# Optimization experiments

Hardware: AMD Instinct MI355X
Metric: run time of the kernel (lower is better)

Reference implementation:

```python
import jax, jax.numpy as jnp
import numpy as np
from jax import lax

N = 100000      # number of nodes (== ninput)
E = 3200000     # number of edges per adjacency
NHID = 128
EPS = 1e-12     # torch F.normalize eps


def spmm(src, dst, w, x):
    # sparse adj @ x : out[i] = sum_{e: dst[e]==i} w[e] * x[src[e]]
    return jax.ops.segment_sum(w[:, None] * x[src], dst, num_segments=N)


def l2norm(x):
    # F.normalize(x, p=2, dim=1)
    n = jnp.sqrt(jnp.sum(x * x, axis=1, keepdims=True))
    return x / jnp.maximum(n, EPS)


def mlp(x, L1, bl1, L2, bl2, L3, bl3):
    # dropout == 0.0 -> identity; chunking is a memory optimization, same math
    h = jax.nn.relu(x @ L1 + bl1)
    h = jax.nn.relu(h @ L2 + bl2)
    return h @ L3 + bl3  # [N, 1]


def setup_inputs() -> dict:
    key = jax.random.key(0)
    ks = jax.random.split(key, 32)
    d = {}
    d["adj1_src"] = jax.random.randint(ks[0], (E,), 0, N, dtype=jnp.int32)
    d["adj1_dst"] = jax.random.randint(ks[1], (E,), 0, N, dtype=jnp.int32)
    d["adj1_w"] = jax.random.uniform(ks[2], (E,), dtype=jnp.float32)
    d["adj2_src"] = jax.random.randint(ks[3], (E,), 0, N, dtype=jnp.int32)
    d["adj2_dst"] = jax.random.randint(ks[4], (E,), 0, N, dtype=jnp.int32)
    d["adj2_w"] = jax.random.uniform(ks[5], (E,), dtype=jnp.float32)
    d["W1"] = jax.random.normal(ks[6], (N, NHID), dtype=jnp.float32) * 0.05
    d["b1"] = jnp.zeros((NHID,), jnp.float32)
    for i, k in zip(range(2, 7), ks[7:12]):
        d[f"W{i}"] = jax.random.normal(k, (NHID, NHID), dtype=jnp.float32) * (1.0 / np.sqrt(NHID))
        d[f"b{i}"] = jnp.zeros((NHID,), jnp.float32)
    d["L1"] = jax.random.normal(ks[12], (NHID, 2 * NHID), dtype=jnp.float32) * (1.0 / np.sqrt(NHID))
    d["bl1"] = jnp.zeros((2 * NHID,), jnp.float32)
    d["L2"] = jax.random.normal(ks[13], (2 * NHID, 2 * NHID), dtype=jnp.float32) * (1.0 / np.sqrt(2 * NHID))
    d["bl2"] = jnp.zeros((2 * NHID,), jnp.float32)
    d["L3"] = jax.random.normal(ks[14], (2 * NHID, 1), dtype=jnp.float32) * (1.0 / np.sqrt(2 * NHID))
    d["bl3"] = jnp.zeros((1,), jnp.float32)
    return d


def reference(adj1_src, adj1_dst, adj1_w, adj2_src, adj2_dst, adj2_w,
              W1, b1, W2, b2, W3, b3, W4, b4, W5, b5, W6, b6,
              L1, bl1, L2, bl2, L3, bl3):
    def branch(src, dst, w):
        x1 = l2norm(jax.nn.relu(spmm(src, dst, w, W1) + b1))
        x2 = l2norm(jax.nn.relu(spmm(src, dst, w, x1 @ W2) + b2))
        x3 = l2norm(jax.nn.relu(spmm(src, dst, w, x2 @ W3) + b3))
        x4 = l2norm(jax.nn.relu(spmm(src, dst, w, x3 @ W4) + b4))
        x5 = l2norm(jax.nn.relu(spmm(src, dst, w, x4 @ W5) + b5))
        x6 = jax.nn.relu(spmm(src, dst, w, x5 @ W6) + b6)
        x7 = lax.stop_gradient(x1 + x2 + x3 + x4 + x5 + x6)  # .detach()
        s = jnp.zeros((N, 1), jnp.float32)
        for xi in (x1, x2, x3, x4, x5):  # computed under torch.no_grad()
            s = s + lax.stop_gradient(mlp(xi, L1, bl1, L2, bl2, L3, bl3))
        s = s + mlp(x6, L1, bl1, L2, bl2, L3, bl3)
        s = s + mlp(x7, L1, bl1, L2, bl2, L3, bl3)
        return s / 7.0

    score1 = branch(adj1_src, adj1_dst, adj1_w)
    score2 = branch(adj2_src, adj2_dst, adj2_w)
    return score1 * score2
```

## Files before the change

### kernel.cpp

```cpp
#include <hip/hip_runtime.h>

#define NN 100000
#define NE 3200000
#define HID 128
#define NNH ((size_t)NN * HID)

typedef __attribute__((ext_vector_type(8))) _Float16 f16x8;
typedef __attribute__((ext_vector_type(4))) _Float16 f16x4;
typedef __attribute__((ext_vector_type(4))) float f32x4;

#define SWZ(row, k) ((k) ^ (((row) & 7) << 3))

__global__ void zero_k(int* p, int n) {
    int i = blockIdx.x * 256 + threadIdx.x;
    if (i < n) p[i] = 0;
}

__global__ void hist_k(const int* __restrict__ dst, int* __restrict__ cnt) {
    int e = blockIdx.x * 256 + threadIdx.x;
    if (e < NE) atomicAdd(&cnt[dst[e]], 1);
}

__global__ __launch_bounds__(1024) void scanA_k(int* __restrict__ rowptr, int* __restrict__ bsum, int n) {
    __shared__ int wsum[16];
    int tid = threadIdx.x;
    int lane = tid & 63, wid = tid >> 6;
    int idx = blockIdx.x * 1024 + tid;
    int v = (idx < n) ? rowptr[idx] : 0;
    int s = v;
#pragma unroll
    for (int o = 1; o < 64; o <<= 1) {
        int t = __shfl_up(s, o, 64);
        if (lane >= o) s += t;
    }
    if (lane == 63) wsum[wid] = s;
    __syncthreads();
    if (wid == 0) {
        int ws = (lane < 16) ? wsum[lane] : 0;
#pragma unroll
        for (int o = 1; o < 16; o <<= 1) {
            int t = __shfl_up(ws, o, 64);
            if (lane >= o) ws += t;
        }
        if (lane < 16) wsum[lane] = ws;
    }
    __syncthreads();
    int woff = (wid == 0) ? 0 : wsum[wid - 1];
    if (idx < n) rowptr[idx] = woff + s - v;
    if (tid == 0) bsum[blockIdx.x] = wsum[15];
}

__global__ void scanB_k(int* __restrict__ bsum, int* __restrict__ rowptr, int nb, int n) {
    if (threadIdx.x == 0) {
        int run = 0;
        for (int i = 0; i < nb; ++i) {
            int t = bsum[i];
            bsum[i] = run;
            run += t;
        }
        rowptr[n] = run;
    }
}

__global__ void scanC_k(int* __restrict__ rowptr, int* __restrict__ cursor,
                        const int* __restrict__ bsum, int n) {
    int idx = blockIdx.x * 256 + threadIdx.x;
    if (idx < n) {
        int v = rowptr[idx] + bsum[idx >> 10];
        rowptr[idx] = v;
        cursor[idx] = v;
    }
}

__global__ void scatter_k(const int* __restrict__ src, const int* __restrict__ dst,
                          const float* __restrict__ w, int* __restrict__ cursor,
                          unsigned* __restrict__ ep) {
    int e = blockIdx.x * 256 + threadIdx.x;
    if (e < NE) {
        int d = dst[e];
        int pos = atomicAdd(&cursor[d], 1);
        ushort hb = __builtin_bit_cast(ushort, (_Float16)w[e]);
        ep[pos] = ((unsigned)src[e] << 15) | (unsigned)hb;
    }
}

__global__ void convT_k(const float* __restrict__ W, _Float16* __restrict__ WT, int K, int N) {
    int idx = blockIdx.x * 256 + threadIdx.x;
    if (idx < K * N) {
        int k = idx / N, n = idx % N;
        WT[n * K + k] = (_Float16)W[idx];
    }
}

__global__ void conv4_k(const float* __restrict__ A, _Float16* __restrict__ B, int n4) {
    int i = blockIdx.x * 256 + threadIdx.x;
    if (i < n4) {
        float4 v = ((const float4*)A)[i];
        f16x4 h;
        h.x = (_Float16)v.x; h.y = (_Float16)v.y; h.z = (_Float16)v.z; h.w = (_Float16)v.w;
        ((f16x4*)B)[i] = h;
    }
}

template <bool EPI>
__global__ void spmm_k(const _Float16* __restrict__ x, const int* __restrict__ rowptr,
                       const unsigned* __restrict__ ep, const float* __restrict__ bias,
                       _Float16* __restrict__ outx) {
    int row = blockIdx.x * 4 + (threadIdx.x >> 6);
    int l = threadIdx.x & 63;
    int q = l >> 4, li = l & 15;
    if (row >= NN) return;
    int e0 = rowptr[row], e1 = rowptr[row + 1];
    float acc[8] = {};
#pragma unroll 4
    for (int e = e0 + q; e < e1; e += 4) {
        unsigned r = ep[e];
        int s = r >> 15;
        float w = (float)__builtin_bit_cast(_Float16, (ushort)(r & 0x7FFFu));
        f16x8 v = *(const f16x8*)(x + (size_t)s * HID + li * 8);
#pragma unroll
        for (int j = 0; j < 8; ++j) acc[j] += w * (float)v[j];
    }
#pragma unroll
    for (int j = 0; j < 8; ++j) {
        acc[j] += __shfl_xor(acc[j], 16, 64);
        acc[j] += __shfl_xor(acc[j], 32, 64);
    }
    if (EPI) {
        const float4* bp = (const float4*)(bias + li * 8);
        float4 b0 = bp[0], b1 = bp[1];
        acc[0] = fmaxf(acc[0] + b0.x, 0.f); acc[1] = fmaxf(acc[1] + b0.y, 0.f);
        acc[2] = fmaxf(acc[2] + b0.z, 0.f); acc[3] = fmaxf(acc[3] + b0.w, 0.f);
        acc[4] = fmaxf(acc[4] + b1.x, 0.f); acc[5] = fmaxf(acc[5] + b1.y, 0.f);
        acc[6] = fmaxf(acc[6] + b1.z, 0.f); acc[7] = fmaxf(acc[7] + b1.w, 0.f);
        float ss = 0.f;
#pragma unroll
        for (int j = 0; j < 8; ++j) ss += acc[j] * acc[j];
        ss += __shfl_xor(ss, 1, 64);
        ss += __shfl_xor(ss, 2, 64);
        ss += __shfl_xor(ss, 4, 64);
        ss += __shfl_xor(ss, 8, 64);
        float sc = 1.0f / fmaxf(sqrtf(ss), 1e-12f);
#pragma unroll
        for (int j = 0; j < 8; ++j) acc[j] *= sc;
    }
    if (q == 0) {
        f16x8 ho;
#pragma unroll
        for (int j = 0; j < 8; ++j) ho[j] = (_Float16)acc[j];
        *(f16x8*)(outx + (size_t)row * HID + li * 8) = ho;
    }
}

template <bool NORM>
__global__ __launch_bounds__(256) void trans_mlp_k(
    const _Float16* __restrict__ Y,
    const _Float16* __restrict__ WT,
    const float* __restrict__ bw,
    _Float16* __restrict__ Xo,
    const _Float16* __restrict__ L1T, const float* __restrict__ bl1,
    const _Float16* __restrict__ L2T, const float* __restrict__ bl2,
    const float* __restrict__ L3, const float* __restrict__ bl3,
    float* __restrict__ sacc) {
    __shared__ _Float16 Xs[64][128];
    __shared__ _Float16 H1s[64][256];
    __shared__ float red[4][64];
    int t = threadIdx.x;
    int w = t >> 6, l = t & 63;
    int g = l >> 4, li = l & 15;
    int rowBase = blockIdx.x * 64;

#pragma unroll
    for (int i = 0; i < 4; ++i) {
        int idx = t + i * 256;
        int r = idx >> 4, c8 = idx & 15;
        int gr = rowBase + r;
        f16x8 v = (gr < NN) ? *(const f16x8*)(Y + (size_t)gr * 128 + c8 * 8)
                            : (f16x8)(_Float16)0.f;
        *(f16x8*)&Xs[r][SWZ(r, c8 * 8)] = v;
    }
    __syncthreads();

    int cW = w * 32;
    f32x4 accw[4][2] = {};
#pragma unroll
    for (int ks = 0; ks < 4; ++ks) {
        int kb = ks * 32 + g * 8;
        f16x8 a[4];
#pragma unroll
        for (int mt = 0; mt < 4; ++mt) {
            int r = mt * 16 + li;
            a[mt] = *(const f16x8*)&Xs[r][SWZ(r, kb)];
        }
#pragma unroll
        for (int nt = 0; nt < 2; ++nt) {
            f16x8 b = *(const f16x8*)(WT + (size_t)(cW + nt * 16 + li) * 128 + kb);
#pragma unroll
            for (int mt = 0; mt < 4; ++mt)
                accw[mt][nt] = __builtin_amdgcn_mfma_f32_16x16x32_f16(a[mt], b, accw[mt][nt], 0, 0, 0);
        }
    }
    float vv[4][2][4];
    float b0 = bw[cW + li], b1v = bw[cW + 16 + li];
#pragma unroll
    for (int mt = 0; mt < 4; ++mt)
#pragma unroll
        for (int r4 = 0; r4 < 4; ++r4) {
            vv[mt][0][r4] = fmaxf(accw[mt][0][r4] + b0, 0.f);
            vv[mt][1][r4] = fmaxf(accw[mt][1][r4] + b1v, 0.f);
        }
    if (NORM) {
#pragma unroll
        for (int mt = 0; mt < 4; ++mt)
#pragma unroll
            for (int r4 = 0; r4 < 4; ++r4) {
                float ps = vv[mt][0][r4] * vv[mt][0][r4] + vv[mt][1][r4] * vv[mt][1][r4];
                ps += __shfl_xor(ps, 1, 64);
                ps += __shfl_xor(ps, 2, 64);
                ps += __shfl_xor(ps, 4, 64);
                ps += __shfl_xor(ps, 8, 64);
                if (li == 0) red[w][mt * 16 + g * 4 + r4] = ps;
            }
        __syncthreads();
        if (t < 64) {
            float s = red[0][t] + red[1][t] + red[2][t] + red[3][t];
            red[0][t] = 1.f / fmaxf(sqrtf(s), 1e-12f);
        }
        __syncthreads();
    } else {
        __syncthreads();
    }
#pragma unroll
    for (int mt = 0; mt < 4; ++mt)
#pragma unroll
        for (int r4 = 0; r4 < 4; ++r4) {
            int row = mt * 16 + g * 4 + r4;
            float sc = NORM ? red[0][row] : 1.f;
            _Float16 h0 = (_Float16)(vv[mt][0][r4] * sc);
            _Float16 h1 = (_Float16)(vv[mt][1][r4] * sc);
            Xs[row][SWZ(row, cW + li)] = h0;
            Xs[row][SWZ(row, cW + 16 + li)] = h1;
            int gr = rowBase + row;
            if (gr < NN) {
                Xo[(size_t)gr * 128 + cW + li] = h0;
                Xo[(size_t)gr * 128 + cW + 16 + li] = h1;
            }
        }
    __syncthreads();

    int cM = w * 64;
    f32x4 acc[4][4] = {};
#pragma unroll
    for (int ks = 0; ks < 4; ++ks) {
        int kb = ks * 32 + g * 8;
        f16x8 a[4];
#pragma unroll
        for (int mt = 0; mt < 4; ++mt) {
            int r = mt * 16 + li;
            a[mt] = *(const f16x8*)&Xs[r][SWZ(r, kb)];
        }
#pragma unroll
        for (int nt = 0; nt < 4; ++nt) {
            int n = cM + nt * 16 + li;
            f16x8 b = *(const f16x8*)(L1T + (size_t)n * 128 + kb);
#pragma unroll
            for (int mt = 0; mt < 4; ++mt)
                acc[mt][nt] = __builtin_amdgcn_mfma_f32_16x16x32_f16(a[mt], b, acc[mt][nt], 0, 0, 0);
        }
    }
#pragma unroll
    for (int nt = 0; nt < 4; ++nt) {
        int col = cM + nt * 16 + li;
        float bb = bl1[col];
#pragma unroll
        for (int mt = 0; mt < 4; ++mt)
#pragma unroll
            for (int r4 = 0; r4 < 4; ++r4) {
                int row = mt * 16 + g * 4 + r4;
                H1s[row][SWZ(row, col)] = (_Float16)fmaxf(acc[mt][nt][r4] + bb, 0.f);
            }
    }
    __syncthreads();

    f32x4 acc2[4][4] = {};
#pragma unroll
    for (int ks = 0; ks < 8; ++ks) {
        int kb = ks * 32 + g * 8;
        f16x8 a[4];
#pragma unroll
        for (int mt = 0; mt < 4; ++mt) {
            int r = mt * 16 + li;
            a[mt] = *(const f16x8*)&H1s[r][SWZ(r, kb)];
        }
#pragma unroll
        for (int nt = 0; nt < 4; ++nt) {
            int n = cM + nt * 16 + li;
            f16x8 b = *(const f16x8*)(L2T + (size_t)n * 256 + kb);
#pragma unroll
            for (int mt = 0; mt < 4; ++mt)
                acc2[mt][nt] = __builtin_amdgcn_mfma_f32_16x16x32_f16(a[mt], b, acc2[mt][nt], 0, 0, 0);
        }
    }
    float part[4][4] = {};
#pragma unroll
    for (int nt = 0; nt < 4; ++nt) {
        int col = cM + nt * 16 + li;
        float bb = bl2[col];
        float l3v = L3[col];
#pragma unroll
        for (int mt = 0; mt < 4; ++mt)
#pragma unroll
            for (int r4 = 0; r4 < 4; ++r4)
                part[mt][r4] += fmaxf(acc2[mt][nt][r4] + bb, 0.f) * l3v;
    }
#pragma unroll
    for (int mt = 0; mt < 4; ++mt)
#pragma unroll
        for (int r4 = 0; r4 < 4; ++r4) {
            float p = part[mt][r4];
            p += __shfl_xor(p, 1, 64);
            p += __shfl_xor(p, 2, 64);
            p += __shfl_xor(p, 4, 64);
            p += __shfl_xor(p, 8, 64);
            if (li == 0) red[w][mt * 16 + g * 4 + r4] = p;
        }
    __syncthreads();
    if (t < 64) {
        int gr = rowBase + t;
        if (gr < NN)
            sacc[gr] += red[0][t] + red[1][t] + red[2][t] + red[3][t] + bl3[0];
    }
}

template <bool SUM6, bool INIT>
__global__ __launch_bounds__(256) void mlp_fused_k(
    const _Float16* __restrict__ X,
    const _Float16* __restrict__ L1T, const float* __restrict__ bl1,
    const _Float16* __restrict__ L2T, const float* __restrict__ bl2,
    const float* __restrict__ L3, const float* __restrict__ bl3,
    float* __restrict__ sacc) {
    __shared__ _Float16 Xs[64][128];
    __shared__ _Float16 H1s[64][256];
    __shared__ float red[4][64];
    int t = threadIdx.x;
    int w = t >> 6, l = t & 63;
    int g = l >> 4, li = l & 15;
    int rowBase = blockIdx.x * 64;

#pragma unroll
    for (int i = 0; i < 4; ++i) {
        int idx = t + i * 256;
        int r = idx >> 4, c8 = idx & 15;
        int gr = rowBase + r;
        if (SUM6) {
            float s[8] = {};
            if (gr < NN) {
#pragma unroll
                for (int l6 = 0; l6 < 6; ++l6) {
                    f16x8 v = *(const f16x8*)(X + (size_t)l6 * NNH + (size_t)gr * HID + c8 * 8);
#pragma unroll
                    for (int j = 0; j < 8; ++j) s[j] += (float)v[j];
                }
            }
            f16x8 hv;
#pragma unroll
            for (int j = 0; j < 8; ++j) hv[j] = (_Float16)s[j];
            *(f16x8*)&Xs[r][SWZ(r, c8 * 8)] = hv;
        } else {
            f16x8 v = (gr < NN) ? *(const f16x8*)(X + (size_t)gr * HID + c8 * 8)
                                : (f16x8)(_Float16)0.f;
            *(f16x8*)&Xs[r][SWZ(r, c8 * 8)] = v;
        }
    }
    __syncthreads();

    int cM = w * 64;
    f32x4 acc[4][4] = {};
#pragma unroll
    for (int ks = 0; ks < 4; ++ks) {
        int kb = ks * 32 + g * 8;
        f16x8 a[4];
#pragma unroll
        for (int mt = 0; mt < 4; ++mt) {
            int r = mt * 16 + li;
            a[mt] = *(const f16x8*)&Xs[r][SWZ(r, kb)];
        }
#pragma unroll
        for (int nt = 0; nt < 4; ++nt) {
            int n = cM + nt * 16 + li;
            f16x8 b = *(const f16x8*)(L1T + (size_t)n * 128 + kb);
#pragma unroll
            for (int mt = 0; mt < 4; ++mt)
                acc[mt][nt] = __builtin_amdgcn_mfma_f32_16x16x32_f16(a[mt], b, acc[mt][nt], 0, 0, 0);
        }
    }
#pragma unroll
    for (int nt = 0; nt < 4; ++nt) {
        int col = cM + nt * 16 + li;
        float bb = bl1[col];
#pragma unroll
        for (int mt = 0; mt < 4; ++mt)
#pragma unroll
            for (int r4 = 0; r4 < 4; ++r4) {
                int row = mt * 16 + g * 4 + r4;
                H1s[row][SWZ(row, col)] = (_Float16)fmaxf(acc[mt][nt][r4] + bb, 0.f);
            }
    }
    __syncthreads();

    f32x4 acc2[4][4] = {};
#pragma unroll
    for (int ks = 0; ks < 8; ++ks) {
        int kb = ks * 32 + g * 8;
        f16x8 a[4];
#pragma unroll
        for (int mt = 0; mt < 4; ++mt) {
            int r = mt * 16 + li;
            a[mt] = *(const f16x8*)&H1s[r][SWZ(r, kb)];
        }
#pragma unroll
        for (int nt = 0; nt < 4; ++nt) {
            int n = cM + nt * 16 + li;
            f16x8 b = *(const f16x8*)(L2T + (size_t)n * 256 + kb);
#pragma unroll
            for (int mt = 0; mt < 4; ++mt)
                acc2[mt][nt] = __builtin_amdgcn_mfma_f32_16x16x32_f16(a[mt], b, acc2[mt][nt], 0, 0, 0);
        }
    }
    float part[4][4] = {};
#pragma unroll
    for (int nt = 0; nt < 4; ++nt) {
        int col = cM + nt * 16 + li;
        float bb = bl2[col];
        float l3v = L3[col];
#pragma unroll
        for (int mt = 0; mt < 4; ++mt)
#pragma unroll
            for (int r4 = 0; r4 < 4; ++r4)
                part[mt][r4] += fmaxf(acc2[mt][nt][r4] + bb, 0.f) * l3v;
    }
#pragma unroll
    for (int mt = 0; mt < 4; ++mt)
#pragma unroll
        for (int r4 = 0; r4 < 4; ++r4) {
            float p = part[mt][r4];
            p += __shfl_xor(p, 1, 64);
            p += __shfl_xor(p, 2, 64);
            p += __shfl_xor(p, 4, 64);
            p += __shfl_xor(p, 8, 64);
            if (li == 0) red[w][mt * 16 + g * 4 + r4] = p;
        }
    __syncthreads();
    if (t < 64) {
        int gr = rowBase + t;
        if (gr < NN) {
            float s = red[0][t] + red[1][t] + red[2][t] + red[3][t] + bl3[0];
            if (INIT) sacc[gr] = s; else sacc[gr] += s;
        }
    }
}

__global__ void score_store_k(const float* __restrict__ sacc, float* __restrict__ dst) {
    int i = blockIdx.x * 256 + threadIdx.x;
    if (i < NN) dst[i] = sacc[i] * (1.f / 7.f);
}

__global__ void final_mul_k(const float* __restrict__ sacc, const float* __restrict__ score1,
                            float* __restrict__ out) {
    int i = blockIdx.x * 256 + threadIdx.x;
    if (i < NN) out[i] = score1[i] * (sacc[i] * (1.f / 7.f));
}

extern "C" void kernel_launch(void* const* d_in, const int* in_sizes, int n_in,
                              void* d_out, int out_size, void* d_ws, size_t ws_size,
                              hipStream_t stream) {
    const int* asrc[2] = {(const int*)d_in[0], (const int*)d_in[3]};
    const int* adst[2] = {(const int*)d_in[1], (const int*)d_in[4]};
    const float* aw[2] = {(const float*)d_in[2], (const float*)d_in[5]};
    const float* W1 = (const float*)d_in[6];
    const float* b1 = (const float*)d_in[7];
    const float* Wk[5] = {(const float*)d_in[8], (const float*)d_in[10], (const float*)d_in[12],
                          (const float*)d_in[14], (const float*)d_in[16]};
    const float* bk[5] = {(const float*)d_in[9], (const float*)d_in[11], (const float*)d_in[13],
                          (const float*)d_in[15], (const float*)d_in[17]};
    const float* L1 = (const float*)d_in[18];
    const float* bl1 = (const float*)d_in[19];
    const float* L2 = (const float*)d_in[20];
    const float* bl2 = (const float*)d_in[21];
    const float* L3 = (const float*)d_in[22];
    const float* bl3 = (const float*)d_in[23];
    float* out = (float*)d_out;

    char* p = (char*)d_ws;
    _Float16* L1T = (_Float16*)p; p += 65536;
    _Float16* L2T = (_Float16*)p; p += 131072;
    _Float16* WkT = (_Float16*)p; p += 163840;
    _Float16* W1h = (_Float16*)p; p += NNH * 2;
    _Float16* tmp = (_Float16*)p; p += NNH * 2;
    _Float16* xbuf = (_Float16*)p; p += 6 * NNH * 2;
    float* sacc = (float*)p; p += (size_t)NN * 4;
    float* score1 = (float*)p; p += (size_t)NN * 4;
    unsigned* ep = (unsigned*)p; p += (size_t)NE * 4;
    int* rowptr = (int*)p; p += (size_t)(NN + 1) * 4;
    int* cursor = (int*)p; p += (size_t)NN * 4;
    int* bsum = (int*)p; p += 512;

    const int GE = (NE + 255) / 256;
    const int GN = (NN + 255) / 256;
    const int GS = (NN + 3) / 4;
    const int GM = (NN + 63) / 64;
    const int NB = (NN + 1023) / 1024;

    convT_k<<<(128 * 256 + 255) / 256, 256, 0, stream>>>(L1, L1T, 128, 256);
    convT_k<<<(256 * 256 + 255) / 256, 256, 0, stream>>>(L2, L2T, 256, 256);
    for (int l = 0; l < 5; ++l)
        convT_k<<<(128 * 128 + 255) / 256, 256, 0, stream>>>(Wk[l], WkT + (size_t)l * 16384, 128, 128);
    conv4_k<<<(NN * HID / 4 + 255) / 256, 256, 0, stream>>>(W1, W1h, NN * HID / 4);

    for (int br = 0; br < 2; ++br) {
        zero_k<<<GN, 256, 0, stream>>>(rowptr, NN + 1);
        hist_k<<<GE, 256, 0, stream>>>(adst[br], rowptr);
        scanA_k<<<NB, 1024, 0, stream>>>(rowptr, bsum, NN);
        scanB_k<<<1, 64, 0, stream>>>(bsum, rowptr, NB, NN);
        scanC_k<<<GN, 256, 0, stream>>>(rowptr, cursor, bsum, NN);
        scatter_k<<<GE, 256, 0, stream>>>(asrc[br], adst[br], aw[br], cursor, ep);

        spmm_k<true><<<GS, 256, 0, stream>>>(W1h, rowptr, ep, b1, xbuf);
        mlp_fused_k<false, true><<<GM, 256, 0, stream>>>(xbuf, L1T, bl1, L2T, bl2, L3, bl3, sacc);

        for (int l = 0; l < 5; ++l) {
            spmm_k<false><<<GS, 256, 0, stream>>>(xbuf + (size_t)l * NNH, rowptr, ep, b1, tmp);
            _Float16* xo = xbuf + (size_t)(l + 1) * NNH;
            if (l < 4)
                trans_mlp_k<true><<<GM, 256, 0, stream>>>(tmp, WkT + (size_t)l * 16384, bk[l], xo,
                                                          L1T, bl1, L2T, bl2, L3, bl3, sacc);
            else
                trans_mlp_k<false><<<GM, 256, 0, stream>>>(tmp, WkT + (size_t)l * 16384, bk[l], xo,
                                                           L1T, bl1, L2T, bl2, L3, bl3, sacc);
        }

        mlp_fused_k<true, false><<<GM, 256, 0, stream>>>(xbuf, L1T, bl1, L2T, bl2, L3, bl3, sacc);

        if (br == 0)
            score_store_k<<<GN, 256, 0, stream>>>(sacc, score1);
        else
            final_mul_k<<<GN, 256, 0, stream>>>(sacc, score1, out);
    }
}
```

Measured before the change: 2.797 ms.

## Replace atomic CSR scatter with two-pass LDS-bucketed scatter

Edge scattering into CSR order is split into two kernels. The first bins edges by coarse destination bucket in shared memory and flushes 32-record chunks to an intermediate array with coalesced writes. The second does a per-bucket counting sort into the final edge array. The aim is to replace random global atomics and scattered writes with localized ones, at the cost of an extra pass over 8-byte records and heavy LDS use.

```diff
diff --git a/kernel.cpp b/kernel.cpp
--- a/kernel.cpp
+++ b/kernel.cpp
@@ -4,10 +4,14 @@
 #define NE 3200000
 #define HID 128
 #define NNH ((size_t)NN * HID)
+#define BSH 9
+#define NBUCK ((NN + (1 << BSH) - 1) >> BSH)
+#define CAP 36
 
 typedef __attribute__((ext_vector_type(8))) _Float16 f16x8;
 typedef __attribute__((ext_vector_type(4))) _Float16 f16x4;
 typedef __attribute__((ext_vector_type(4))) float f32x4;
+typedef unsigned long long u64;
 
 #define SWZ(row, k) ((k) ^ (((row) & 7) << 3))
 
@@ -62,25 +66,111 @@
     }
 }
 
-__global__ void scanC_k(int* __restrict__ rowptr, int* __restrict__ cursor,
+__global__ void scanC_k(int* __restrict__ rowptr, int* __restrict__ gcur,
                         const int* __restrict__ bsum, int n) {
     int idx = blockIdx.x * 256 + threadIdx.x;
     if (idx < n) {
         int v = rowptr[idx] + bsum[idx >> 10];
         rowptr[idx] = v;
-        cursor[idx] = v;
-    }
-}
-
-__global__ void scatter_k(const int* __restrict__ src, const int* __restrict__ dst,
-                          const float* __restrict__ w, int* __restrict__ cursor,
-                          unsigned* __restrict__ ep) {
-    int e = blockIdx.x * 256 + threadIdx.x;
-    if (e < NE) {
-        int d = dst[e];
-        int pos = atomicAdd(&cursor[d], 1);
-        ushort hb = __builtin_bit_cast(ushort, (_Float16)w[e]);
-        ep[pos] = ((unsigned)src[e] << 15) | (unsigned)hb;
+        if ((idx & ((1 << BSH) - 1)) == 0) gcur[idx >> BSH] = v;
+    }
+}
+
+__global__ __launch_bounds__(256) void bucketA_k(const int* __restrict__ src,
+                                                 const int* __restrict__ dst,
+                                                 const float* __restrict__ w,
+                                                 int* __restrict__ gcur,
+                                                 u64* __restrict__ im) {
+    __shared__ u64 buf[NBUCK][CAP];
+    __shared__ int cnt[NBUCK];
+    int tid = threadIdx.x;
+    int wid = tid >> 6, lane = tid & 63;
+    for (int b = tid; b < NBUCK; b += 256) cnt[b] = 0;
+    __syncthreads();
+    for (int base = blockIdx.x * 256; base < NE; base += gridDim.x * 256) {
+        int e = base + tid;
+        if (e < NE) {
+            int d = dst[e];
+            ushort hb = __builtin_bit_cast(ushort, (_Float16)w[e]);
+            unsigned packed = ((unsigned)src[e] << 15) | (unsigned)hb;
+            u64 rec = ((u64)(unsigned)d << 32) | packed;
+            int bk = d >> BSH;
+            int pos = atomicAdd(&cnt[bk], 1);
+            if (pos < CAP) {
+                buf[bk][pos] = rec;
+            } else {
+                int gp = atomicAdd(&gcur[bk], 1);
+                im[gp] = rec;
+                atomicSub(&cnt[bk], 1);
+            }
+        }
+        __syncthreads();
+        for (int b = wid; b < NBUCK; b += 4) {
+            int nrec = cnt[b];
+            int n32 = nrec & ~31;
+            if (n32 > 0) {
+                int gbase;
+                if (lane == 0) gbase = atomicAdd(&gcur[b], n32);
+                gbase = __shfl(gbase, 0, 64);
+                for (int r = lane; r < n32; r += 64) im[gbase + r] = buf[b][r];
+                int rem = nrec - n32;
+                for (int r = lane; r < rem; r += 64) buf[b][r] = buf[b][n32 + r];
+                if (lane == 0) cnt[b] = rem;
+            }
+        }
+        __syncthreads();
+    }
+    for (int b = wid; b < NBUCK; b += 4) {
+        int nrec = cnt[b];
+        if (nrec > 0) {
+            int gbase;
+            if (lane == 0) gbase = atomicAdd(&gcur[b], nrec);
+            gbase = __shfl(gbase, 0, 64);
+            for (int r = lane; r < nrec; r += 64) im[gbase + r] = buf[b][r];
+        }
+    }
+}
+
+__global__ __launch_bounds__(256) void bucketB_k(const int* __restrict__ rowptr,
+                                                 const u64* __restrict__ im,
+                                                 unsigned* __restrict__ ep) {
+    __shared__ int cnt[1 << BSH];
+    __shared__ int wsum[4];
+    int b = blockIdx.x;
+    int r0 = b << BSH;
+    int r1 = r0 + (1 << BSH); if (r1 > NN) r1 = NN;
+    int s0 = rowptr[r0], s1 = rowptr[r1];
+    int n = s1 - s0;
+    int tid = threadIdx.x;
+    int wid = tid >> 6, lane = tid & 63;
+    cnt[tid] = 0; cnt[tid + 256] = 0;
+    __syncthreads();
+    for (int i = tid; i < n; i += 256)
+        atomicAdd(&cnt[(int)(im[s0 + i] >> 32) - r0], 1);
+    __syncthreads();
+    int a0 = cnt[2 * tid], a1 = cnt[2 * tid + 1];
+    int p = a0 + a1;
+    int s = p;
+#pragma unroll
+    for (int o = 1; o < 64; o <<= 1) {
+        int t = __shfl_up(s, o, 64);
+        if (lane >= o) s += t;
+    }
+    if (lane == 63) wsum[wid] = s;
+    __syncthreads();
+    int woff = 0;
+    if (wid > 0) woff = wsum[0];
+    if (wid > 1) woff += wsum[1];
+    if (wid > 2) woff += wsum[2];
+    int excl = woff + s - p;
+    __syncthreads();
+    cnt[2 * tid] = s0 + excl;
+    cnt[2 * tid + 1] = s0 + excl + a0;
+    __syncthreads();
+    for (int i = tid; i < n; i += 256) {
+        u64 rec = im[s0 + i];
+        int pos = atomicAdd(&cnt[(int)(rec >> 32) - r0], 1);
+        ep[pos] = (unsigned)rec;
     }
 }
 
@@ -154,10 +244,8 @@
 
 template <bool NORM>
 __global__ __launch_bounds__(256) void trans_mlp_k(
-    const _Float16* __restrict__ Y,
-    const _Float16* __restrict__ WT,
-    const float* __restrict__ bw,
-    _Float16* __restrict__ Xo,
+    const _Float16* __restrict__ Y, const _Float16* __restrict__ WT,
+    const float* __restrict__ bw, _Float16* __restrict__ Xo,
     const _Float16* __restrict__ L1T, const float* __restrict__ bl1,
     const _Float16* __restrict__ L2T, const float* __restrict__ bl2,
     const float* __restrict__ L3, const float* __restrict__ bl3,
@@ -502,8 +590,9 @@
     float* score1 = (float*)p; p += (size_t)NN * 4;
     unsigned* ep = (unsigned*)p; p += (size_t)NE * 4;
     int* rowptr = (int*)p; p += (size_t)(NN + 1) * 4;
-    int* cursor = (int*)p; p += (size_t)NN * 4;
+    int* gcur = (int*)p; p += (size_t)NBUCK * 4;
     int* bsum = (int*)p; p += 512;
+    u64* im = (u64*)tmp;
 
     const int GE = (NE + 255) / 256;
     const int GN = (NN + 255) / 256;
@@ -522,8 +611,9 @@
         hist_k<<<GE, 256, 0, stream>>>(adst[br], rowptr);
         scanA_k<<<NB, 1024, 0, stream>>>(rowptr, bsum, NN);
         scanB_k<<<1, 64, 0, stream>>>(bsum, rowptr, NB, NN);
-        scanC_k<<<GN, 256, 0, stream>>>(rowptr, cursor, bsum, NN);
-        scatter_k<<<GE, 256, 0, stream>>>(asrc[br], adst[br], aw[br], cursor, ep);
+        scanC_k<<<GN, 256, 0, stream>>>(rowptr, gcur, bsum, NN);
+        bucketA_k<<<512, 256, 0, stream>>>(asrc[br], adst[br], aw[br], gcur, im);
+        bucketB_k<<<NBUCK, 256, 0, stream>>>(rowptr, im, ep);
 
         spmm_k<true><<<GS, 256, 0, stream>>>(W1h, rowptr, ep, b1, xbuf);
         mlp_fused_k<false, true><<<GM, 256, 0, stream>>>(xbuf, L1T, bl1, L2T, bl2, L3, bl3, sacc);
```

Result: slower. 3.486 ms (+24.6%).
